# Optimization experiments

Measured on AMD Instinct MI355X. Metric: run time of the kernel, lower is better.

The kernel has to match this reference:

```python
import jax, jax.numpy as jnp
import numpy as np

B, N, C_IN, C_OUT = 2, 512, 64, 64  # mid_dim == out_dim
EPS = 1e-5

def _bn(x, g, b):
    # PyTorch BatchNorm1d in training mode: biased batch stats over axis 0 of [M, C]
    mu = x.mean(axis=0)
    var = x.var(axis=0)
    return (x - mu) * jax.lax.rsqrt(var + EPS) * g + b

def setup_inputs() -> dict:
    key = jax.random.key(0)
    ks = jax.random.split(key, 16)
    s = 0.05
    return {
        "pos": jax.random.normal(ks[0], (B, N, 3), jnp.float32),
        "c_features": jax.random.normal(ks[1], (B, N, C_IN), jnp.float32),
        "Wq": jax.random.normal(ks[2], (C_OUT, C_IN), jnp.float32) * s,
        "bq": jnp.zeros((C_OUT,), jnp.float32),
        "Wk": jax.random.normal(ks[3], (C_OUT, C_IN), jnp.float32) * s,
        "bk": jnp.zeros((C_OUT,), jnp.float32),
        "Wv": jax.random.normal(ks[4], (C_OUT, C_IN), jnp.float32) * s,
        "bv": jnp.zeros((C_OUT,), jnp.float32),
        "Wp1": jax.random.normal(ks[5], (3, 3), jnp.float32) * s,
        "bp1": jnp.zeros((3,), jnp.float32),
        "g_p": jnp.ones((3,), jnp.float32),
        "b_p": jnp.zeros((3,), jnp.float32),
        "Wp2": jax.random.normal(ks[6], (C_OUT, 3), jnp.float32) * s,
        "bp2": jnp.zeros((C_OUT,), jnp.float32),
        "g_w": jnp.ones((C_OUT,), jnp.float32),
        "b_w": jnp.zeros((C_OUT,), jnp.float32),
        "Ww1": jax.random.normal(ks[7], (C_OUT, C_OUT), jnp.float32) * s,
        "bw1": jnp.zeros((C_OUT,), jnp.float32),
        "Ww2": jax.random.normal(ks[8], (C_OUT, C_OUT), jnp.float32) * s,
        "bw2": jnp.zeros((C_OUT,), jnp.float32),
    }

def reference(pos, c_features, Wq, bq, Wk, bk, Wv, bv, Wp1, bp1, g_p, b_p, Wp2, bp2, g_w, b_w, Ww1, bw1, Ww2, bw2):
    b, n = pos.shape[0], pos.shape[1]
    q = c_features @ Wq.T + bq                       # [B,N,Cmid]
    k = c_features @ Wk.T + bk
    v = c_features @ Wv.T + bv                       # [B,N,Cout]
    rel = pos[:, :, None, :] - pos[:, None, :, :]    # [B,N,N,3]
    h = rel.reshape(-1, 3) @ Wp1.T + bp1             # [B*N*N,3]
    h = jax.nn.relu(_bn(h, g_p, b_p))
    delta = (h @ Wp2.T + bp2).reshape(b, n, n, -1)   # [B,N,N,Cmid]
    qk = q[:, :, None, :] - k[:, None, :, :] + delta # [B,N,N,Cmid]
    h2 = _bn(qk.reshape(-1, qk.shape[-1]), g_w, b_w)
    h2 = jax.nn.relu(h2)
    h2 = jax.nn.relu(h2 @ Ww1.T + bw1)
    w = (h2 @ Ww2.T + bw2).reshape(b, n, n, -1)      # [B,N,N,Cout]
    attn = jax.nn.softmax(w, axis=2)                 # softmax over j
    out = jnp.sum(attn * (v[:, None, :, :] + delta), axis=2)  # [B,N,Cout]
    return out
```

## Files before the change

### kernel.cpp

```cpp
#include <hip/hip_runtime.h>
#include <stdint.h>
#include <stddef.h>

#define DEV __device__ __forceinline__

typedef __attribute__((ext_vector_type(4))) float f32x4;
typedef __attribute__((ext_vector_type(8))) short bf16x8;

union FragU { bf16x8 f; uint32_t u[4]; };

DEV uint32_t pk_bf16(float a, float b) {
  uint32_t d;
  asm("v_cvt_pk_bf16_f32 %0, %1, %2" : "=v"(d) : "v"(a), "v"(b));
  return d;
}

DEV uint16_t f2bf(float x) {
  uint32_t u = __float_as_uint(x);
  u += 0x7fffu + ((u >> 16) & 1u);
  return (uint16_t)(u >> 16);
}

__launch_bounds__(256)
__global__ void kAll(const float* __restrict__ cf, const float* __restrict__ pos,
                     const float* __restrict__ Wq, const float* __restrict__ Wk,
                     const float* __restrict__ Wv, const float* __restrict__ bq,
                     const float* __restrict__ bk, const float* __restrict__ bv,
                     const float* __restrict__ Ww1, const float* __restrict__ Ww2,
                     const float* __restrict__ Wp1, const float* __restrict__ g_p,
                     const float* __restrict__ b_p, const float* __restrict__ bp2,
                     float* __restrict__ qo, float* __restrict__ ko,
                     float* __restrict__ vT, uint16_t* __restrict__ W1bf,
                     uint16_t* __restrict__ W2bf, float* __restrict__ hpa,
                     float* __restrict__ Mpart, float* __restrict__ XPp,
                     float* __restrict__ SNp) {
  const int bid = blockIdx.x, t = threadIdx.x;

  __shared__ float cfl[4][64];
  __shared__ __align__(16) f32x4 X[512];
  __shared__ float U[64][64];
  __shared__ float redr[64][4][4];
  __shared__ float mred[256][6];
  __shared__ float mred2[64][6];
  __shared__ float rfin[64][4];
  __shared__ float redn[256][2];
  __shared__ float wred[4][2][9];
  __shared__ float a1L[3];

  if (bid < 256) {
    const int rr = t >> 6, c = t & 63;
    const int r0 = bid * 4;
    cfl[rr][c] = cf[(size_t)(r0 + rr) * 64 + c];
    __syncthreads();
    const int bn = r0 + rr;
    const float* wqr = Wq + c * 64;
    const float* wkr = Wk + c * 64;
    const float* wvr = Wv + c * 64;
    float aq = bq[c], ak = bk[c], av = bv[c] + bp2[c];
#pragma unroll 8
    for (int kk = 0; kk < 64; ++kk) {
      const float f = cfl[rr][kk];
      aq = fmaf(f, wqr[kk], aq);
      ak = fmaf(f, wkr[kk], ak);
      av = fmaf(f, wvr[kk], av);
    }
    qo[(size_t)bn * 64 + c] = aq;
    ko[(size_t)bn * 64 + c] = ak;
    vT[((size_t)(bn >> 9) * 64 + c) * 512 + (bn & 511)] = av;
  } else if (bid == 256) {
    const float L2E = 1.4426950408889634f;
    for (int idx = t; idx < 8192; idx += 256) {
      const int m = idx >> 12;
      const int r = idx & 4095;
      const int f = r >> 9;
      const int l = (r >> 3) & 63;
      const int e = r & 7;
      const int nt = f >> 1, ks = f & 1, lm = l & 15, lq = l >> 4;
      const int row = 16 * nt + lm, col = 8 * lq + 32 * ks + e;
      const float src = m ? (Ww2[row * 64 + col] * L2E) : Ww1[row * 64 + col];
      (m ? W2bf : W1bf)[r] = f2bf(src);
    }
  } else {
    const int sb = bid - 257;
    const int s = sb >> 4, b = (sb >> 3) & 1, chunk = sb & 7;
    const int r0g = b * 512 + chunk * 64;

    {
      const int w = t >> 6, c = t & 63;
      const float* wr = (s ? Wk : Wq) + c * 64;
      const float bias = s ? bk[c] : (bq[c] + bp2[c]);
      f32x4 wreg[16];
#pragma unroll
      for (int kv = 0; kv < 16; ++kv) wreg[kv] = *(const f32x4*)(wr + kv * 4);
      for (int m = 0; m < 16; ++m) {
        const int row = w * 16 + m;
        const f32x4* cfr = (const f32x4*)(cf + (size_t)(r0g + row) * 64);
        float a0 = bias, a1v = 0.f, a2v = 0.f, a3v = 0.f;
#pragma unroll
        for (int kv = 0; kv < 16; ++kv) {
          const f32x4 f = cfr[kv];
          a0 = fmaf(f.x, wreg[kv].x, a0);
          a1v = fmaf(f.y, wreg[kv].y, a1v);
          a2v = fmaf(f.z, wreg[kv].z, a2v);
          a3v = fmaf(f.w, wreg[kv].w, a3v);
        }
        U[row][c] = (a0 + a1v) + (a2v + a3v);
      }
    }

    {
      const int l = t & 63, wid = t >> 6;
      for (int b2 = 0; b2 < 2; ++b2) {
        float s9[9] = {0, 0, 0, 0, 0, 0, 0, 0, 0};
        for (int r = 0; r < 2; ++r) {
          const int row = t + 256 * r;
          const float* p = pos + (size_t)(b2 * 512 + row) * 3;
          const float p0 = p[0], p1 = p[1], p2 = p[2];
          s9[0] += p0; s9[1] += p1; s9[2] += p2;
          s9[3] += p0 * p0; s9[4] += p0 * p1; s9[5] += p0 * p2;
          s9[6] += p1 * p1; s9[7] += p1 * p2; s9[8] += p2 * p2;
        }
#pragma unroll
        for (int a = 0; a < 9; ++a) {
          float v = s9[a];
          v += __shfl_xor(v, 1);  v += __shfl_xor(v, 2);  v += __shfl_xor(v, 4);
          v += __shfl_xor(v, 8);  v += __shfl_xor(v, 16); v += __shfl_xor(v, 32);
          s9[a] = v;
        }
        if (l == 0) {
#pragma unroll
          for (int a = 0; a < 9; ++a) wred[wid][b2][a] = s9[a];
        }
      }
    }
    __syncthreads();
    if (t == 0) {
      float C[6] = {0, 0, 0, 0, 0, 0};
      const float invM = 1.0f / 524288.0f;
      for (int b2 = 0; b2 < 2; ++b2) {
        float acc9[9];
#pragma unroll
        for (int a = 0; a < 9; ++a)
          acc9[a] = wred[0][b2][a] + wred[1][b2][a] + wred[2][b2][a] + wred[3][b2][a];
        C[0] += 1024.f * acc9[3] - 2.f * acc9[0] * acc9[0];
        C[1] += 1024.f * acc9[4] - 2.f * acc9[0] * acc9[1];
        C[2] += 1024.f * acc9[5] - 2.f * acc9[0] * acc9[2];
        C[3] += 1024.f * acc9[6] - 2.f * acc9[1] * acc9[1];
        C[4] += 1024.f * acc9[7] - 2.f * acc9[1] * acc9[2];
        C[5] += 1024.f * acc9[8] - 2.f * acc9[2] * acc9[2];
      }
      for (int a = 0; a < 6; ++a) C[a] *= invM;
      for (int tt = 0; tt < 3; ++tt) {
        const float w0 = Wp1[tt * 3 + 0], w1 = Wp1[tt * 3 + 1], w2 = Wp1[tt * 3 + 2];
        const float var = w0 * w0 * C[0] + w1 * w1 * C[3] + w2 * w2 * C[5]
                        + 2.f * (w0 * w1 * C[1] + w0 * w2 * C[2] + w1 * w2 * C[4]);
        a1L[tt] = g_p[tt] * rsqrtf(var + 1e-5f);
      }
    }
    __syncthreads();

    {
      const float a10 = a1L[0], a11 = a1L[1], a12 = a1L[2];
      const float w00 = Wp1[0], w01 = Wp1[1], w02 = Wp1[2];
      const float w10 = Wp1[3], w11 = Wp1[4], w12 = Wp1[5];
      const float w20 = Wp1[6], w21 = Wp1[7], w22 = Wp1[8];
      for (int r = 0; r < 2; ++r) {
        const int row = t + 256 * r;
        const float* p = pos + (size_t)(b * 512 + row) * 3;
        const float p0 = p[0], p1 = p[1], p2 = p[2];
        f32x4 v;
        v.x = a10 * (w00 * p0 + w01 * p1 + w02 * p2);
        v.y = a11 * (w10 * p0 + w11 * p1 + w12 * p2);
        v.z = a12 * (w20 * p0 + w21 * p1 + w22 * p2);
        v.w = 0.f;
        if (s == 0 && chunk == 0)
          *(f32x4*)(hpa + (size_t)(b * 512 + row) * 4) = v;
        if (s) { v.x = -v.x; v.y = -v.y; v.z = -v.z; }
        X[row] = v;
      }
    }
    __syncthreads();

    {
      const int al = t >> 2, qr = t & 3;
      const int a = chunk * 64 + al;
      const f32x4 xa = X[a];
      const float base0 = xa.x + b_p[0], base1 = xa.y + b_p[1], base2 = xa.z + b_p[2];
      float r0 = 0, r1 = 0, r2 = 0;
      float m00 = 0, m01 = 0, m02 = 0, m11 = 0, m12 = 0, m22 = 0;
#pragma unroll 8
      for (int jj = qr * 128; jj < qr * 128 + 128; ++jj) {
        const f32x4 xj = X[jj];
        const float h0 = fmaxf(0.f, base0 - xj.x);
        const float h1 = fmaxf(0.f, base1 - xj.y);
        const float h2 = fmaxf(0.f, base2 - xj.z);
        r0 += h0; r1 += h1; r2 += h2;
        if (s == 0) {
          m00 = fmaf(h0, h0, m00); m01 = fmaf(h0, h1, m01); m02 = fmaf(h0, h2, m02);
          m11 = fmaf(h1, h1, m11); m12 = fmaf(h1, h2, m12); m22 = fmaf(h2, h2, m22);
        }
      }
      redr[al][qr][0] = r0; redr[al][qr][1] = r1; redr[al][qr][2] = r2; redr[al][qr][3] = 0.f;
      mred[t][0] = m00; mred[t][1] = m01; mred[t][2] = m02;
      mred[t][3] = m11; mred[t][4] = m12; mred[t][5] = m22;
    }
    __syncthreads();

    if (t < 64) {
      float sx = 0, sy = 0, sz = 0;
#pragma unroll
      for (int p = 0; p < 4; ++p) { sx += redr[t][p][0]; sy += redr[t][p][1]; sz += redr[t][p][2]; }
      rfin[t][0] = sx; rfin[t][1] = sy; rfin[t][2] = sz; rfin[t][3] = 0.f;
      if (s == 0) {
#pragma unroll
        for (int cc = 0; cc < 6; ++cc)
          mred2[t][cc] = mred[t][cc] + mred[t + 64][cc] + mred[t + 128][cc] + mred[t + 192][cc];
      }
    }
    __syncthreads();

    if (s == 0 && t < 6) {
      float m = 0.f;
      for (int p = 0; p < 64; ++p) m += mred2[p][t];
      Mpart[sb * 12 + t] = m;
    }
    if (s == 0 && t >= 64 && t < 67) {
      const int tt = t - 64;
      float v = 0.f;
#pragma unroll 8
      for (int a = 0; a < 64; ++a) v += rfin[a][tt];
      Mpart[sb * 12 + 6 + tt] = v;
    }
    if (t < 192) {
      const int c = t & 63, tt = t >> 6;
      float xp = 0.f;
#pragma unroll 8
      for (int a = 0; a < 64; ++a) xp = fmaf(U[a][c], rfin[a][tt], xp);
      if (s) xp = -xp;
      XPp[((size_t)sb * 3 + tt) * 64 + c] = xp;
    }
    {
      const int c = t & 63, g = t >> 6;
      float su = 0.f, su2 = 0.f;
#pragma unroll
      for (int r = 0; r < 16; ++r) {
        const float v = U[g * 16 + r][c];
        su += v;
        su2 = fmaf(v, v, su2);
      }
      redn[t][0] = su; redn[t][1] = su2;
    }
    __syncthreads();
    if (t < 64) {
      float a0 = 0.f, a1v = 0.f;
#pragma unroll
      for (int p = 0; p < 4; ++p) { a0 += redn[t + 64 * p][0]; a1v += redn[t + 64 * p][1]; }
      SNp[((size_t)sb * 2 + 0) * 64 + t] = a0;
      SNp[((size_t)sb * 2 + 1) * 64 + t] = a1v;
    }
  }
}

__launch_bounds__(256)
__global__ void k3_main(const float* __restrict__ q, const float* __restrict__ kk_,
                        const float* __restrict__ vT, const float* __restrict__ hpa,
                        const float* __restrict__ Mpart, const float* __restrict__ XPp,
                        const float* __restrict__ SNp, const float* __restrict__ g_w,
                        const float* __restrict__ b_w,
                        const uint16_t* __restrict__ W1bf, const uint16_t* __restrict__ W2bf,
                        const float* __restrict__ bp2, const float* __restrict__ Wp2,
                        const float* __restrict__ b_p, const float* __restrict__ bw1g,
                        const float* __restrict__ bw2g, float* __restrict__ out) {
  const int bid = blockIdx.x;
  const int b = bid >> 9, i = bid & 511;
  const int t = threadIdx.x;
  const int wid = t >> 6, l = t & 63;
  const int lm = l & 15, lq = l >> 4;

  __shared__ __align__(16) uint16_t W1l[4096];
  __shared__ __align__(16) uint16_t W2l[4096];
  __shared__ __align__(16) uint16_t H2[4][16][76];
  __shared__ __align__(16) float P0[64];
  __shared__ __align__(16) float a2s[64];
  __shared__ __align__(16) float Pts[3][64];
  __shared__ __align__(16) float comb[4][64][2];
  __shared__ float xps[4][3][64];
  __shared__ float sns[4][2][64];
  __shared__ float msh[12];

  {
    *(bf16x8*)(&W1l[t * 16])     = *(const bf16x8*)(W1bf + t * 16);
    *(bf16x8*)(&W1l[t * 16 + 8]) = *(const bf16x8*)(W1bf + t * 16 + 8);
    *(bf16x8*)(&W2l[t * 16])     = *(const bf16x8*)(W2bf + t * 16);
    *(bf16x8*)(&W2l[t * 16 + 8]) = *(const bf16x8*)(W2bf + t * 16 + 8);
  }

  {
    const int qd = t >> 6, c = t & 63;
    float x0 = 0, x1 = 0, x2 = 0, s0 = 0, s1 = 0;
#pragma unroll
    for (int p = 0; p < 8; ++p) {
      const int blk = qd * 8 + p;
      x0 += XPp[((size_t)blk * 3 + 0) * 64 + c];
      x1 += XPp[((size_t)blk * 3 + 1) * 64 + c];
      x2 += XPp[((size_t)blk * 3 + 2) * 64 + c];
      s0 += SNp[((size_t)blk * 2 + 0) * 64 + c];
      s1 += SNp[((size_t)blk * 2 + 1) * 64 + c];
    }
    xps[qd][0][c] = x0; xps[qd][1][c] = x1; xps[qd][2][c] = x2;
    sns[qd][0][c] = s0; sns[qd][1][c] = s1;
    if (t < 12) {
      float m = 0.f;
#pragma unroll
      for (int p = 0; p < 16; ++p) m += Mpart[p * 12 + t];
      msh[t] = m;
    }
  }
  __syncthreads();

  if (t < 64) {
    const int c = t;
    const float URd0 = xps[0][0][c] + xps[1][0][c] + xps[2][0][c] + xps[3][0][c];
    const float URd1 = xps[0][1][c] + xps[1][1][c] + xps[2][1][c] + xps[3][1][c];
    const float URd2 = xps[0][2][c] + xps[1][2][c] + xps[2][2][c] + xps[3][2][c];
    const float Su0 = sns[0][0][c], Su20 = sns[0][1][c];
    const float Su1 = sns[1][0][c], Su21 = sns[1][1][c];
    const float Sk0 = sns[2][0][c], Sk20 = sns[2][1][c];
    const float Sk1 = sns[3][0][c], Sk21 = sns[3][1][c];
    const float P0t = Wp2[c * 3 + 0], P1t = Wp2[c * 3 + 1], P2t = Wp2[c * 3 + 2];
    const float Nf = 512.f, invM = 1.f / 524288.f;
    float S1 = Nf * (Su0 - Sk0) + Nf * (Su1 - Sk1);
    const float Q2 = Nf * Su20 - 2.f * Su0 * Sk0 + Nf * Sk20
                   + Nf * Su21 - 2.f * Su1 * Sk1 + Nf * Sk21;
    const float Xc = P0t * URd0 + P1t * URd1 + P2t * URd2;
    S1 += P0t * msh[6] + P1t * msh[7] + P2t * msh[8];
    const float Hm = P0t * P0t * msh[0] + 2.f * P0t * P1t * msh[1] + 2.f * P0t * P2t * msh[2]
                   + P1t * P1t * msh[3] + 2.f * P1t * P2t * msh[4] + P2t * P2t * msh[5];
    const float E1 = S1 * invM;
    const float E2 = (Q2 + 2.f * Xc + Hm) * invM;
    const float var = E2 - E1 * E1;
    const float A2 = g_w[c] * rsqrtf(var + 1e-5f);
    const float be2 = b_w[c] - E1 * A2;
    a2s[c] = A2;
    P0[c] = fmaf(A2, q[(size_t)(b * 512 + i) * 64 + c] + bp2[c], be2);
    Pts[0][c] = A2 * P0t;
    Pts[1][c] = A2 * P1t;
    Pts[2][c] = A2 * P2t;
  }

  const f32x4 hi = *(const f32x4*)(hpa + (size_t)(b * 512 + i) * 4);
  const float bb0 = b_p[0], bb1 = b_p[1], bb2 = b_p[2];
  const float LOG2E = 1.4426950408889634f;

  float bw1r[4], bw2l[4], wpa[4], wpb[4], wpc[4];
#pragma unroll
  for (int nt = 0; nt < 4; ++nt) {
    const int c = 16 * nt + lm;
    bw1r[nt] = bw1g[c];
    bw2l[nt] = bw2g[c] * LOG2E;
    wpa[nt] = Wp2[c * 3 + 0];
    wpb[nt] = Wp2[c * 3 + 1];
    wpc[nt] = Wp2[c * 3 + 2];
  }

  float l_[4] = {0.f, 0.f, 0.f, 0.f};
  float acc_[4] = {0.f, 0.f, 0.f, 0.f};

  __syncthreads();

  const float* kbase = kk_ + (size_t)(b * 512) * 64;
  const float* hbase = hpa + (size_t)(b * 512) * 4;
  const float* vTb = vT + (size_t)b * 64 * 512;

  f32x4 kvA[2][2];
  {
    const int j0 = wid * 16 + lm;
#pragma unroll
    for (int ks = 0; ks < 2; ++ks) {
      kvA[ks][0] = *(const f32x4*)(kbase + (size_t)j0 * 64 + 32 * ks + 8 * lq);
      kvA[ks][1] = *(const f32x4*)(kbase + (size_t)j0 * 64 + 32 * ks + 8 * lq + 4);
    }
  }

  for (int it = 0; it < 8; ++it) {
    const int jb = it * 64 + wid * 16;
    const int j = jb + lm;
    const int j2 = jb + 4 * lq;

    f32x4 kvN[2][2];
    if (it < 7) {
      const int jn = j + 64;
#pragma unroll
      for (int ks = 0; ks < 2; ++ks) {
        kvN[ks][0] = *(const f32x4*)(kbase + (size_t)jn * 64 + 32 * ks + 8 * lq);
        kvN[ks][1] = *(const f32x4*)(kbase + (size_t)jn * 64 + 32 * ks + 8 * lq + 4);
      }
    }

    const f32x4 hj = *(const f32x4*)(hbase + j * 4);
    f32x4 hjr[4];
#pragma unroll
    for (int r = 0; r < 4; ++r) hjr[r] = *(const f32x4*)(hbase + (j2 + r) * 4);
    f32x4 vv[4];
#pragma unroll
    for (int nt = 0; nt < 4; ++nt)
      vv[nt] = *(const f32x4*)(vTb + (size_t)(16 * nt + lm) * 512 + j2);

    const float h0 = fmaxf(0.f, hi.x - hj.x + bb0);
    const float h1 = fmaxf(0.f, hi.y - hj.y + bb1);
    const float h2v = fmaxf(0.f, hi.z - hj.z + bb2);

    FragU A1[2];
#pragma unroll
    for (int ks = 0; ks < 2; ++ks) {
      const int c0 = 32 * ks + 8 * lq;
      f32x4 pv[2], av[2], t0[2], t1[2], t2[2];
      pv[0] = *(const f32x4*)(P0 + c0);        pv[1] = *(const f32x4*)(P0 + c0 + 4);
      av[0] = *(const f32x4*)(a2s + c0);       av[1] = *(const f32x4*)(a2s + c0 + 4);
      t0[0] = *(const f32x4*)(&Pts[0][c0]);    t0[1] = *(const f32x4*)(&Pts[0][c0 + 4]);
      t1[0] = *(const f32x4*)(&Pts[1][c0]);    t1[1] = *(const f32x4*)(&Pts[1][c0 + 4]);
      t2[0] = *(const f32x4*)(&Pts[2][c0]);    t2[1] = *(const f32x4*)(&Pts[2][c0 + 4]);
      float x[8];
#pragma unroll
      for (int e = 0; e < 8; ++e) {
        const int hh = e >> 2, e4 = e & 3;
        float xv = pv[hh][e4] - av[hh][e4] * kvA[ks][hh][e4];
        xv = fmaf(t0[hh][e4], h0, xv);
        xv = fmaf(t1[hh][e4], h1, xv);
        xv = fmaf(t2[hh][e4], h2v, xv);
        x[e] = fmaxf(0.f, xv);
      }
      A1[ks].u[0] = pk_bf16(x[0], x[1]);
      A1[ks].u[1] = pk_bf16(x[2], x[3]);
      A1[ks].u[2] = pk_bf16(x[4], x[5]);
      A1[ks].u[3] = pk_bf16(x[6], x[7]);
    }

    f32x4 d1[4];
#pragma unroll
    for (int nt = 0; nt < 4; ++nt) {
      FragU b0, b1;
      b0.f = *(const bf16x8*)(&W1l[((nt * 2 + 0) * 64 + l) * 8]);
      b1.f = *(const bf16x8*)(&W1l[((nt * 2 + 1) * 64 + l) * 8]);
      f32x4 z = {bw1r[nt], bw1r[nt], bw1r[nt], bw1r[nt]};
      z = __builtin_amdgcn_mfma_f32_16x16x32_bf16(A1[0].f, b0.f, z, 0, 0, 0);
      z = __builtin_amdgcn_mfma_f32_16x16x32_bf16(A1[1].f, b1.f, z, 0, 0, 0);
      d1[nt] = z;
    }

    uint16_t (*h2w)[76] = H2[wid];
#pragma unroll
    for (int nt = 0; nt < 4; ++nt) {
      const uint32_t u01 = pk_bf16(fmaxf(0.f, d1[nt][0]), fmaxf(0.f, d1[nt][1]));
      const uint32_t u23 = pk_bf16(fmaxf(0.f, d1[nt][2]), fmaxf(0.f, d1[nt][3]));
      const int col = 16 * nt + lm;
      h2w[4 * lq + 0][col] = (uint16_t)(u01 & 0xffffu);
      h2w[4 * lq + 1][col] = (uint16_t)(u01 >> 16);
      h2w[4 * lq + 2][col] = (uint16_t)(u23 & 0xffffu);
      h2w[4 * lq + 3][col] = (uint16_t)(u23 >> 16);
    }

    FragU A2[2];
    A2[0].f = *(const bf16x8*)(&h2w[lm][8 * lq]);
    A2[1].f = *(const bf16x8*)(&h2w[lm][32 + 8 * lq]);

    f32x4 d2[4];
#pragma unroll
    for (int nt = 0; nt < 4; ++nt) {
      FragU b0, b1;
      b0.f = *(const bf16x8*)(&W2l[((nt * 2 + 0) * 64 + l) * 8]);
      b1.f = *(const bf16x8*)(&W2l[((nt * 2 + 1) * 64 + l) * 8]);
      f32x4 z = {bw2l[nt], bw2l[nt], bw2l[nt], bw2l[nt]};
      z = __builtin_amdgcn_mfma_f32_16x16x32_bf16(A2[0].f, b0.f, z, 0, 0, 0);
      z = __builtin_amdgcn_mfma_f32_16x16x32_bf16(A2[1].f, b1.f, z, 0, 0, 0);
      d2[nt] = z;
    }

    float hr0[4], hr1[4], hr2[4];
#pragma unroll
    for (int r = 0; r < 4; ++r) {
      hr0[r] = fmaxf(0.f, hi.x - hjr[r].x + bb0);
      hr1[r] = fmaxf(0.f, hi.y - hjr[r].y + bb1);
      hr2[r] = fmaxf(0.f, hi.z - hjr[r].z + bb2);
    }

#pragma unroll
    for (int nt = 0; nt < 4; ++nt) {
      float p[4], val[4];
#pragma unroll
      for (int r = 0; r < 4; ++r) {
        p[r] = __builtin_amdgcn_exp2f(d2[nt][r]);
        float v0 = vv[nt][r];
        v0 = fmaf(wpa[nt], hr0[r], v0);
        v0 = fmaf(wpb[nt], hr1[r], v0);
        v0 = fmaf(wpc[nt], hr2[r], v0);
        val[r] = v0;
      }
      l_[nt] += (p[0] + p[1]) + (p[2] + p[3]);
      float a = acc_[nt];
      a = fmaf(p[0], val[0], a);
      a = fmaf(p[1], val[1], a);
      a = fmaf(p[2], val[2], a);
      a = fmaf(p[3], val[3], a);
      acc_[nt] = a;
    }

    if (it < 7) {
#pragma unroll
      for (int ks = 0; ks < 2; ++ks) {
        kvA[ks][0] = kvN[ks][0];
        kvA[ks][1] = kvN[ks][1];
      }
    }
  }

#pragma unroll
  for (int nt = 0; nt < 4; ++nt) {
    l_[nt] += __shfl_xor(l_[nt], 16);
    acc_[nt] += __shfl_xor(acc_[nt], 16);
    l_[nt] += __shfl_xor(l_[nt], 32);
    acc_[nt] += __shfl_xor(acc_[nt], 32);
  }
  if (lq == 0) {
#pragma unroll
    for (int nt = 0; nt < 4; ++nt) {
      comb[wid][16 * nt + lm][0] = l_[nt];
      comb[wid][16 * nt + lm][1] = acc_[nt];
    }
  }
  __syncthreads();
  if (t < 64) {
    float L = 0.f, A = 0.f;
#pragma unroll
    for (int w = 0; w < 4; ++w) {
      L += comb[w][t][0];
      A += comb[w][t][1];
    }
    out[(size_t)(b * 512 + i) * 64 + t] = A / L;
  }
}

extern "C" void kernel_launch(void* const* d_in, const int* in_sizes, int n_in,
                              void* d_out, int out_size, void* d_ws, size_t ws_size,
                              hipStream_t stream) {
  (void)in_sizes; (void)n_in; (void)out_size; (void)ws_size;
  const float* pos = (const float*)d_in[0];
  const float* cf  = (const float*)d_in[1];
  const float* Wq  = (const float*)d_in[2];
  const float* bq  = (const float*)d_in[3];
  const float* Wk  = (const float*)d_in[4];
  const float* bk  = (const float*)d_in[5];
  const float* Wv  = (const float*)d_in[6];
  const float* bv  = (const float*)d_in[7];
  const float* Wp1 = (const float*)d_in[8];
  const float* g_p = (const float*)d_in[10];
  const float* b_p = (const float*)d_in[11];
  const float* Wp2 = (const float*)d_in[12];
  const float* bp2 = (const float*)d_in[13];
  const float* g_w = (const float*)d_in[14];
  const float* b_w = (const float*)d_in[15];
  const float* Ww1 = (const float*)d_in[16];
  const float* bw1 = (const float*)d_in[17];
  const float* Ww2 = (const float*)d_in[18];
  const float* bw2 = (const float*)d_in[19];

  char* ws = (char*)d_ws;
  uint16_t* W1bf = (uint16_t*)(ws + 0);
  uint16_t* W2bf = (uint16_t*)(ws + 8192);
  float*    hpaw = (float*)(ws + 16896);
  float*    qw   = (float*)(ws + 33280);
  float*    kw   = (float*)(ws + 295424);
  float*    vTw  = (float*)(ws + 557568);
  float*    Mpw  = (float*)(ws + 821248);
  float*    XPpw = (float*)(ws + 823040);
  float*    SNpw = (float*)(ws + 847872);

  kAll<<<dim3(289), dim3(256), 0, stream>>>(cf, pos, Wq, Wk, Wv, bq, bk, bv,
                                            Ww1, Ww2, Wp1, g_p, b_p, bp2,
                                            qw, kw, vTw, W1bf, W2bf, hpaw,
                                            Mpw, XPpw, SNpw);
  k3_main<<<dim3(1024), dim3(256), 0, stream>>>(qw, kw, vTw, hpaw, Mpw, XPpw, SNpw,
                                                g_w, b_w, W1bf, W2bf, bp2, Wp2, b_p,
                                                bw1, bw2, (float*)d_out);
}
```

Before: 74.53 us.

## Stage QKV weights transposed in shared memory and raise MFMA wave priority

The QKV projection blocks now each process 8 rows. They stage each weight matrix transposed into padded shared memory so global weight reads are coalesced, and they write vT through an LDS transpose as vectorized stores. This halves the prologue grid and reuses the U buffer for the statistics path. Separately, s_setprio brackets are added around the two MFMA loops in the main kernel to favour waves issuing matrix ops. The extra syncs and serial weight loads add some latency to the small prologue.

```diff
diff --git a/kernel.cpp b/kernel.cpp
--- a/kernel.cpp
+++ b/kernel.cpp
@@ -36,9 +36,8 @@
                      float* __restrict__ SNp) {
   const int bid = blockIdx.x, t = threadIdx.x;
 
-  __shared__ float cfl[4][64];
+  __shared__ __align__(16) float Ush[4160];
   __shared__ __align__(16) f32x4 X[512];
-  __shared__ float U[64][64];
   __shared__ float redr[64][4][4];
   __shared__ float mred[256][6];
   __shared__ float mred2[64][6];
@@ -47,27 +46,46 @@
   __shared__ float wred[4][2][9];
   __shared__ float a1L[3];
 
-  if (bid < 256) {
-    const int rr = t >> 6, c = t & 63;
-    const int r0 = bid * 4;
-    cfl[rr][c] = cf[(size_t)(r0 + rr) * 64 + c];
+  if (bid < 128) {
+    const int c = t & 63, rr = t >> 6;
+    const int r0 = bid * 8;
+    float accq[2], acck[2], accv[2];
+    for (int m = 0; m < 3; ++m) {
+      __syncthreads();
+      const float* Wm = (m == 0) ? Wq : ((m == 1) ? Wk : Wv);
+      for (int idx = t; idx < 4096; idx += 256)
+        Ush[(idx & 63) * 65 + (idx >> 6)] = Wm[idx];
+      __syncthreads();
+#pragma unroll
+      for (int rp = 0; rp < 2; ++rp) {
+        const int row = r0 + rr + 4 * rp;
+        const float* cfr = cf + (size_t)row * 64;
+        float a = 0.f;
+#pragma unroll 8
+        for (int kk = 0; kk < 64; ++kk)
+          a = fmaf(cfr[kk], Ush[kk * 65 + c], a);
+        if (m == 0) accq[rp] = a;
+        else if (m == 1) acck[rp] = a;
+        else accv[rp] = a;
+      }
+    }
+#pragma unroll
+    for (int rp = 0; rp < 2; ++rp) {
+      const int bn = r0 + rr + 4 * rp;
+      qo[(size_t)bn * 64 + c] = accq[rp] + bq[c];
+      ko[(size_t)bn * 64 + c] = acck[rp] + bk[c];
+    }
+    float* vb = (float*)X;
+    const float bvv = bv[c] + bp2[c];
+    vb[c * 12 + rr] = accv[0] + bvv;
+    vb[c * 12 + rr + 4] = accv[1] + bvv;
     __syncthreads();
-    const int bn = r0 + rr;
-    const float* wqr = Wq + c * 64;
-    const float* wkr = Wk + c * 64;
-    const float* wvr = Wv + c * 64;
-    float aq = bq[c], ak = bk[c], av = bv[c] + bp2[c];
-#pragma unroll 8
-    for (int kk = 0; kk < 64; ++kk) {
-      const float f = cfl[rr][kk];
-      aq = fmaf(f, wqr[kk], aq);
-      ak = fmaf(f, wkr[kk], ak);
-      av = fmaf(f, wvr[kk], av);
-    }
-    qo[(size_t)bn * 64 + c] = aq;
-    ko[(size_t)bn * 64 + c] = ak;
-    vT[((size_t)(bn >> 9) * 64 + c) * 512 + (bn & 511)] = av;
-  } else if (bid == 256) {
+    if (t < 128) {
+      const int c2 = t >> 1, hf = t & 1;
+      const f32x4 v = *(const f32x4*)(vb + c2 * 12 + 4 * hf);
+      *(f32x4*)(vT + ((size_t)(r0 >> 9) * 64 + c2) * 512 + (r0 & 511) + 4 * hf) = v;
+    }
+  } else if (bid == 128) {
     const float L2E = 1.4426950408889634f;
     for (int idx = t; idx < 8192; idx += 256) {
       const int m = idx >> 12;
@@ -81,7 +99,7 @@
       (m ? W2bf : W1bf)[r] = f2bf(src);
     }
   } else {
-    const int sb = bid - 257;
+    const int sb = bid - 129;
     const int s = sb >> 4, b = (sb >> 3) & 1, chunk = sb & 7;
     const int r0g = b * 512 + chunk * 64;
 
@@ -104,7 +122,7 @@
           a2v = fmaf(f.z, wreg[kv].z, a2v);
           a3v = fmaf(f.w, wreg[kv].w, a3v);
         }
-        U[row][c] = (a0 + a1v) + (a2v + a3v);
+        Ush[row * 64 + c] = (a0 + a1v) + (a2v + a3v);
       }
     }
 
@@ -235,7 +253,7 @@
       const int c = t & 63, tt = t >> 6;
       float xp = 0.f;
 #pragma unroll 8
-      for (int a = 0; a < 64; ++a) xp = fmaf(U[a][c], rfin[a][tt], xp);
+      for (int a = 0; a < 64; ++a) xp = fmaf(Ush[a * 64 + c], rfin[a][tt], xp);
       if (s) xp = -xp;
       XPp[((size_t)sb * 3 + tt) * 64 + c] = xp;
     }
@@ -244,7 +262,7 @@
       float su = 0.f, su2 = 0.f;
 #pragma unroll
       for (int r = 0; r < 16; ++r) {
-        const float v = U[g * 16 + r][c];
+        const float v = Ush[(g * 16 + r) * 64 + c];
         su += v;
         su2 = fmaf(v, v, su2);
       }
@@ -437,6 +455,7 @@
     }
 
     f32x4 d1[4];
+    __builtin_amdgcn_s_setprio(1);
 #pragma unroll
     for (int nt = 0; nt < 4; ++nt) {
       FragU b0, b1;
@@ -447,6 +466,7 @@
       z = __builtin_amdgcn_mfma_f32_16x16x32_bf16(A1[1].f, b1.f, z, 0, 0, 0);
       d1[nt] = z;
     }
+    __builtin_amdgcn_s_setprio(0);
 
     uint16_t (*h2w)[76] = H2[wid];
 #pragma unroll
@@ -465,6 +485,7 @@
     A2[1].f = *(const bf16x8*)(&h2w[lm][32 + 8 * lq]);
 
     f32x4 d2[4];
+    __builtin_amdgcn_s_setprio(1);
 #pragma unroll
     for (int nt = 0; nt < 4; ++nt) {
       FragU b0, b1;
@@ -475,6 +496,7 @@
       z = __builtin_amdgcn_mfma_f32_16x16x32_bf16(A2[1].f, b1.f, z, 0, 0, 0);
       d2[nt] = z;
     }
+    __builtin_amdgcn_s_setprio(0);
 
     float hr0[4], hr1[4], hr2[4];
 #pragma unroll
@@ -575,7 +597,7 @@
   float*    XPpw = (float*)(ws + 823040);
   float*    SNpw = (float*)(ws + 847872);
 
-  kAll<<<dim3(289), dim3(256), 0, stream>>>(cf, pos, Wq, Wk, Wv, bq, bk, bv,
+  kAll<<<dim3(161), dim3(256), 0, stream>>>(cf, pos, Wq, Wk, Wv, bq, bk, bv,
                                             Ww1, Ww2, Wp1, g_p, b_p, bp2,
                                             qw, kw, vTw, W1bf, W2bf, hpaw,
                                             Mpw, XPpw, SNpw);
```

After: 69.97 us. -6.1%, faster.
